# Optimization experiments

Measured on AMD Instinct MI355X. Metric: run time of the kernel, lower is better.

The kernel has to match this reference:

```python
import jax, jax.numpy as jnp
import numpy as np

B, D, N = 2, 256, 8192   # batch, in_channels, sequence length
CI = 128                 # inter_channels
BN_EPS = 1e-5


def conv1x1(w, b, x):
    # w: (Cout, Cin), b: (Cout,), x: (B, Cin, N) -> (B, Cout, N)
    return jnp.einsum('oc,bcn->bon', w, x) + b[None, :, None]


def maxpool2(x):
    # MaxPool1d(kernel_size=2): (B, C, N) -> (B, C, N//2)
    b, c, n = x.shape
    return x.reshape(b, c, n // 2, 2).max(axis=-1)


def setup_inputs() -> dict:
    key = jax.random.key(0)
    ks = jax.random.split(key, 11)
    s_in = 1.0 / np.sqrt(D)
    s_ci = 1.0 / np.sqrt(CI)
    return {
        'f': jax.random.normal(ks[0], (B, D, N), dtype=jnp.float32),
        'g_w': jax.random.uniform(ks[1], (CI, D), jnp.float32, -s_in, s_in),
        'g_b': jax.random.uniform(ks[2], (CI,), jnp.float32, -s_in, s_in),
        'theta_w': jax.random.uniform(ks[3], (CI, D), jnp.float32, -s_in, s_in),
        'theta_b': jax.random.uniform(ks[4], (CI,), jnp.float32, -s_in, s_in),
        'phi_w': jax.random.uniform(ks[5], (CI, D), jnp.float32, -s_in, s_in),
        'phi_b': jax.random.uniform(ks[6], (CI,), jnp.float32, -s_in, s_in),
        'W_w': jax.random.uniform(ks[7], (D, CI), jnp.float32, -s_ci, s_ci),
        'W_b': jax.random.uniform(ks[8], (D,), jnp.float32, -s_ci, s_ci),
        'bn_gamma': jax.random.normal(ks[9], (D,), dtype=jnp.float32) * 0.1,
        'bn_beta': jax.random.normal(ks[10], (D,), dtype=jnp.float32) * 0.1,
    }


def reference(f, g_w, g_b, theta_w, theta_b, phi_w, phi_b, W_w, W_b, bn_gamma, bn_beta):
    # projections (1x1 convs); g and phi are sub-sampled by maxpool(2)
    g_f = maxpool2(conv1x1(g_w, g_b, f))          # (B, CI, N/2)
    theta_f = conv1x1(theta_w, theta_b, f)        # (B, CI, N)
    phi_f = maxpool2(conv1x1(phi_w, phi_b, f))    # (B, CI, N/2)

    # affinity: theta^T @ phi, softmax over keys (no scale, as in source)
    A = jnp.einsum('bcn,bcm->bnm', theta_f, phi_f)     # (B, N, N/2)
    A = jax.nn.softmax(A, axis=-1)
    y = jnp.einsum('bnm,bcm->bcn', A, g_f)             # (B, CI, N)

    # W: 1x1 conv + BatchNorm1d (training-mode batch stats), residual
    Wy = conv1x1(W_w, W_b, y)                          # (B, D, N)
    mean = Wy.mean(axis=(0, 2), keepdims=True)
    var = Wy.var(axis=(0, 2), keepdims=True)           # biased, like torch BN
    Wy = (Wy - mean) * jax.lax.rsqrt(var + BN_EPS)
    Wy = Wy * bn_gamma[None, :, None] + bn_beta[None, :, None]
    return Wy + f
```

## Files before the change

### kernel.cpp

```cpp
#include <hip/hip_runtime.h>
#include <hip/hip_bf16.h>
#include <math.h>

#define B_ 2
#define D_ 256
#define N_ 8192
#define CI_ 128
#define M_ 4096
#define BN_EPS_ 1e-5f
#define LOG2E_ 1.4426950408889634f

#define GLOBAL_AS __attribute__((address_space(1)))
#define LDS_AS __attribute__((address_space(3)))

#define OFF_WALL 0
#define OFF_THT  65536
#define OFF_PHT  (OFF_THT + 1048576)
#define OFF_GT   (OFF_PHT + 524288)
#define OFF_YP   (OFF_GT  + 524288)
#define OFF_ML   (OFF_YP  + 4194304)
#define OFF_MEAN (OFF_ML + 131072)
#define OFF_RSTD (OFF_MEAN + 256)

typedef __attribute__((ext_vector_type(8))) short bfrag;
typedef __attribute__((ext_vector_type(4))) float f4v;
typedef __attribute__((ext_vector_type(16))) float f16v;
typedef __attribute__((ext_vector_type(4))) short s4v;
typedef __attribute__((ext_vector_type(4))) unsigned u4v;

__device__ inline unsigned short bf16rne(float x) {
    unsigned u = __float_as_uint(x);
    u += 0x7fff + ((u >> 16) & 1);
    return (unsigned short)(u >> 16);
}

__device__ inline float exp2fast(float x) {
    float r;
    asm("v_exp_f32 %0, %1" : "=v"(r) : "v"(x));
    return r;
}

__global__ __launch_bounds__(256) void wconv_kernel(
    const float* __restrict__ gw, const float* __restrict__ tw, const float* __restrict__ pw,
    const float* __restrict__ Ww, short* __restrict__ wall)
{
    int idx = blockIdx.x * 256 + threadIdx.x;
    int which = idx >> 15;
    int rem = idx & 32767;
    const float* src = (which == 0) ? gw : (which == 1) ? tw : (which == 2) ? pw : Ww;
    float v = src[rem];
    if (which == 1) v *= LOG2E_;
    wall[idx] = (short)bf16rne(v);
}

__global__ __launch_bounds__(256, 2) void proj_kernel(
    const float* __restrict__ f, const short* __restrict__ wall,
    const float* __restrict__ tb, const float* __restrict__ gb, const float* __restrict__ pb,
    short* __restrict__ th_t, short* __restrict__ g_t, short* __restrict__ ph_t)
{
    __shared__ short sF[32 * 72];

    const int tid = threadIdx.x;
    const int wave = tid >> 6, lane = tid & 63;
    const int lq = lane & 15, quad = lane >> 4;
    const int b = blockIdx.y;
    const int n0 = blockIdx.x * 32;

    const float* fb = f + (size_t)b * D_ * N_;

    f4v acc[6][2];
#pragma unroll
    for (int ct = 0; ct < 6; ct++)
#pragma unroll
        for (int nf = 0; nf < 2; nf++) acc[ct][nf] = (f4v){0.f, 0.f, 0.f, 0.f};

    const int sn = tid & 31;
    const int sgrp = tid >> 5;

    for (int kc = 0; kc < D_; kc += 64) {
        __syncthreads();
#pragma unroll
        for (int jj = 0; jj < 4; jj++) {
            int dd = kc + sgrp * 8 + 2 * jj;
            float v0 = fb[(size_t)dd * N_ + n0 + sn];
            float v1 = fb[(size_t)(dd + 1) * N_ + n0 + sn];
            unsigned pk = (unsigned)bf16rne(v0) | ((unsigned)bf16rne(v1) << 16);
            *(unsigned*)&sF[sn * 72 + sgrp * 8 + 2 * jj] = pk;
        }
        __syncthreads();

        bfrag afr[6][2], bfr[2][2];
#pragma unroll
        for (int ks = 0; ks < 2; ks++) {
#pragma unroll
            for (int nf = 0; nf < 2; nf++)
                bfr[nf][ks] = *(const bfrag*)&sF[(nf * 16 + lq) * 72 + ks * 32 + quad * 8];
#pragma unroll
            for (int ct = 0; ct < 6; ct++)
                afr[ct][ks] = *(const bfrag*)&wall[(wave * 96 + ct * 16 + lq) * 256 + kc + ks * 32 + quad * 8];
        }
#pragma unroll
        for (int ks = 0; ks < 2; ks++)
#pragma unroll
            for (int ct = 0; ct < 6; ct++) {
                acc[ct][0] = __builtin_amdgcn_mfma_f32_16x16x32_bf16(afr[ct][ks], bfr[0][ks], acc[ct][0], 0, 0, 0);
                acc[ct][1] = __builtin_amdgcn_mfma_f32_16x16x32_bf16(afr[ct][ks], bfr[1][ks], acc[ct][1], 0, 0, 0);
            }
    }

#pragma unroll
    for (int ct = 0; ct < 6; ct++) {
        const int cf = wave * 6 + ct;
#pragma unroll
        for (int nf = 0; nf < 2; nf++) {
            f4v v = acc[ct][nf];
            const int n = n0 + nf * 16 + lq;
            if (cf < 8) {
                const int cb = cf * 16 + quad * 4;
                float pl[4];
#pragma unroll
                for (int r = 0; r < 4; r++) {
                    float o = __shfl_xor(v[r], 1);
                    pl[r] = fmaxf(v[r], o) + gb[cb + r];
                }
                if (!(lq & 1)) {
                    const int m = n >> 1;
#pragma unroll
                    for (int r = 0; r < 4; r++)
                        g_t[((size_t)b * CI_ + cb + r) * M_ + m] = (short)bf16rne(pl[r]);
                }
            } else if (cf < 16) {
                const int cb = (cf - 8) * 16 + quad * 4;
                s4v o;
#pragma unroll
                for (int r = 0; r < 4; r++) o[r] = (short)bf16rne(v[r] + tb[cb + r] * LOG2E_);
                *(s4v*)&th_t[((size_t)b * N_ + n) * CI_ + cb] = o;
            } else {
                const int cb = (cf - 16) * 16 + quad * 4;
                float pl[4];
#pragma unroll
                for (int r = 0; r < 4; r++) {
                    float o = __shfl_xor(v[r], 1);
                    pl[r] = fmaxf(v[r], o) + pb[cb + r];
                }
                if (!(lq & 1)) {
                    const int m = n >> 1;
                    s4v o;
#pragma unroll
                    for (int r = 0; r < 4; r++) o[r] = (short)bf16rne(pl[r]);
                    *(s4v*)&ph_t[((size_t)b * M_ + m) * CI_ + cb] = o;
                }
            }
        }
    }
}

__global__ __launch_bounds__(256, 2) void attn_kernel(
    const short* __restrict__ th_p, const short* __restrict__ ph_p,
    const short* __restrict__ g_p, short* __restrict__ yp, float* __restrict__ ml)
{
    __shared__ short sPh[2][64 * 128];

    const int tid = threadIdx.x;
    const int wave = tid >> 6, lane = tid & 63;
    const int l = lane & 31, h = lane >> 5;

    const int bid = blockIdx.x;
    const int b = bid & 1;
    const int split = (bid >> 1) & 3;
    const int q0 = (bid >> 3) * 128;
    const int qg = q0 + wave * 32 + l;

    const short* thr = th_p + ((size_t)b * N_ + qg) * CI_;
    bfrag tf[8];
#pragma unroll
    for (int s = 0; s < 8; s++)
        tf[s] = *(const bfrag*)&thr[s * 16 + h * 8];

    f16v yacc[4];
#pragma unroll
    for (int ct = 0; ct < 4; ct++)
#pragma unroll
        for (int r = 0; r < 16; r++) yacc[ct][r] = 0.f;
    float mI = -INFINITY, lI = 0.f;

    const short* phg = ph_p + (size_t)b * M_ * CI_;
    const short* gg  = g_p + (size_t)b * CI_ * M_;

    const int k0 = split * 1024;
    const int xm = l & 15;

    const int prow = (lane >> 4);
    const int pslot = lane & 15;

#define STAGE_DMA(BUF, KC)                                                                  \
    do {                                                                                    \
        _Pragma("unroll")                                                                   \
        for (int p = 0; p < 4; p++) {                                                       \
            const int rp = wave * 16 + p * 4 + prow;                     \
            const int cg = pslot ^ (p * 4 + prow);                   \
            __builtin_amdgcn_global_load_lds(                                               \
                (const GLOBAL_AS void*)(phg + (size_t)((KC) + rp) * 128 + cg * 8),          \
                (LDS_AS void*)(&sPh[BUF][(wave * 16 + p * 4) * 128]), 16, 0, 0);            \
        }                                                                                   \
    } while (0)

    STAGE_DMA(0, k0);

    int cur = 0;
    for (int kc = k0; kc < k0 + 1024; kc += 64) {
        __syncthreads();
        const bool nxt = (kc + 64 < k0 + 1024);

        bfrag ga[4][4];
#pragma unroll
        for (int ct = 0; ct < 4; ct++)
#pragma unroll
            for (int s = 0; s < 4; s++)
                ga[ct][s] = *(const bfrag*)&gg[(size_t)(ct * 32 + l) * M_ + kc + s * 16 + h * 8];

        if (nxt) STAGE_DMA(cur ^ 1, kc + 64);
        __builtin_amdgcn_sched_barrier(0);

        f16v sv[2];
        __builtin_amdgcn_s_setprio(1);
#pragma unroll
        for (int kt = 0; kt < 2; kt++) {
            f16v a;
#pragma unroll
            for (int r = 0; r < 16; r++) a[r] = 0.f;
#pragma unroll
            for (int s = 0; s < 8; s++) {
                bfrag pa = *(const bfrag*)&sPh[cur][(kt * 32 + l) * 128 + (((s << 1) | h) ^ xm) * 8];
                a = __builtin_amdgcn_mfma_f32_32x32x16_bf16(pa, tf[s], a, 0, 0, 0);
            }
            sv[kt] = a;
        }
        __builtin_amdgcn_s_setprio(0);

        float mx = fmaxf(sv[0][0], sv[1][0]);
#pragma unroll
        for (int r = 1; r < 16; r++) mx = fmaxf(mx, fmaxf(sv[0][r], sv[1][r]));
        mx = fmaxf(mx, __shfl_xor(mx, 32));

        if (__any(mx > mI + 8.f)) {
            float mnew = fmaxf(mI, mx);
            float al = exp2fast(mI - mnew);
            lI *= al;
#pragma unroll
            for (int ct = 0; ct < 4; ct++)
#pragma unroll
                for (int r = 0; r < 16; r++) yacc[ct][r] *= al;
            mI = mnew;
        }

        float ps = 0.f;
        unsigned pw[16];
#pragma unroll
        for (int kt = 0; kt < 2; kt++)
#pragma unroll
            for (int i = 0; i < 8; i++) {
                const int r = 2 * i;
                float p0 = exp2fast(sv[kt][r] - mI);
                float p1 = exp2fast(sv[kt][r + 1] - mI);
                ps += p0 + p1;
                unsigned pk;
                asm("v_cvt_pk_bf16_f32 %0, %1, %2" : "=v"(pk) : "v"(p0), "v"(p1));
                pw[kt * 8 + (i >> 1) * 2 + (i & 1)] = pk;
            }
        ps += __shfl_xor(ps, 32);
        lI += ps;

        bfrag pf[4];
#pragma unroll
        for (int s = 0; s < 4; s++) {
            const int kt = s >> 1;
            const int iA = kt * 8 + ((2 * s) & 3) * 2;
            const int iB = kt * 8 + ((2 * s + 1) & 3) * 2;
            unsigned A0 = pw[iA], A1 = pw[iA + 1];
            unsigned B0 = pw[iB], B1 = pw[iB + 1];
            unsigned O0 = h ? B0 : A0;
            unsigned O1 = h ? B1 : A1;
            unsigned Xs0 = h ? A0 : B0;
            unsigned Xs1 = h ? A1 : B1;
            unsigned X0 = (unsigned)__shfl_xor((int)Xs0, 32);
            unsigned X1 = (unsigned)__shfl_xor((int)Xs1, 32);
            u4v t;
            t.x = h ? X0 : O0;
            t.y = h ? X1 : O1;
            t.z = h ? O0 : X0;
            t.w = h ? O1 : X1;
            pf[s] = __builtin_bit_cast(bfrag, t);
        }

        __builtin_amdgcn_s_setprio(1);
#pragma unroll
        for (int ct = 0; ct < 4; ct++)
#pragma unroll
            for (int s = 0; s < 4; s++)
                yacc[ct] = __builtin_amdgcn_mfma_f32_32x32x16_bf16(ga[ct][s], pf[s], yacc[ct], 0, 0, 0);
        __builtin_amdgcn_s_setprio(0);

        cur ^= 1;
    }
#undef STAGE_DMA

    short* yb = yp + (((size_t)split * B_ + b) * N_) * CI_;
#pragma unroll
    for (int ct = 0; ct < 4; ct++)
#pragma unroll
        for (int rq = 0; rq < 4; rq++) {
            const int c0 = ct * 32 + 8 * rq + 4 * h;
            s4v o;
#pragma unroll
            for (int j = 0; j < 4; j++) o[j] = (short)bf16rne(yacc[ct][rq * 4 + j]);
            *(s4v*)&yb[(size_t)qg * CI_ + c0] = o;
        }
    if (h == 0) {
        float* mlb = ml + ((split * B_ + b) * 2) * N_;
        mlb[qg] = mI;
        mlb[N_ + qg] = lI;
    }
}

__global__ __launch_bounds__(256) void wy_merge_kernel(
    const short* __restrict__ yp, const float* __restrict__ ml,
    const short* __restrict__ wall2, const float* __restrict__ Wb,
    float* __restrict__ out)
{
    const int tid = threadIdx.x;
    const int wave = tid >> 6, lane = tid & 63;
    const int l = lane & 31, h = lane >> 5;
    const int b = blockIdx.y;
    const int n = blockIdx.x * 32 + l;

    float m[4], lv[4];
#pragma unroll
    for (int sp = 0; sp < 4; sp++) {
        const float* mlb = ml + ((sp * B_ + b) * 2) * N_;
        m[sp] = mlb[n];
        lv[sp] = mlb[N_ + n];
    }
    float mmax = fmaxf(fmaxf(m[0], m[1]), fmaxf(m[2], m[3]));
    float e[4], den = 0.f;
#pragma unroll
    for (int sp = 0; sp < 4; sp++) { e[sp] = exp2fast(m[sp] - mmax); den += lv[sp] * e[sp]; }
    float inv = 1.0f / den;
#pragma unroll
    for (int sp = 0; sp < 4; sp++) e[sp] *= inv;

    bfrag by[8];
#pragma unroll
    for (int s = 0; s < 8; s++) {
        float a[8];
#pragma unroll
        for (int j = 0; j < 8; j++) a[j] = 0.f;
#pragma unroll
        for (int sp = 0; sp < 4; sp++) {
            bfrag yv = *(const bfrag*)&yp[(((size_t)sp * B_ + b) * N_ + n) * CI_ + s * 16 + h * 8];
            u4v u = __builtin_bit_cast(u4v, yv);
#pragma unroll
            for (int p = 0; p < 4; p++) {
                a[2 * p]     = fmaf(e[sp], __uint_as_float(u[p] << 16), a[2 * p]);
                a[2 * p + 1] = fmaf(e[sp], __uint_as_float(u[p] & 0xffff0000u), a[2 * p + 1]);
            }
        }
        u4v pk;
#pragma unroll
        for (int p = 0; p < 4; p++) {
            unsigned r;
            asm("v_cvt_pk_bf16_f32 %0, %1, %2" : "=v"(r) : "v"(a[2 * p]), "v"(a[2 * p + 1]));
            pk[p] = r;
        }
        by[s] = __builtin_bit_cast(bfrag, pk);
    }

    f16v acc[2];
#pragma unroll
    for (int rt = 0; rt < 2; rt++)
#pragma unroll
        for (int r = 0; r < 16; r++) acc[rt][r] = 0.f;

#pragma unroll
    for (int s = 0; s < 8; s++)
#pragma unroll
        for (int rt = 0; rt < 2; rt++) {
            bfrag aw = *(const bfrag*)&wall2[((wave * 2 + rt) * 32 + l) * 128 + s * 16 + h * 8];
            acc[rt] = __builtin_amdgcn_mfma_f32_32x32x16_bf16(aw, by[s], acc[rt], 0, 0, 0);
        }

#pragma unroll
    for (int rt = 0; rt < 2; rt++)
#pragma unroll
        for (int r = 0; r < 16; r++) {
            const int d = (wave * 2 + rt) * 32 + (r & 3) + 8 * (r >> 2) + 4 * h;
            out[((size_t)b * D_ + d) * N_ + n] = acc[rt][r] + Wb[d];
        }
}

__global__ __launch_bounds__(256) void stats_kernel(
    const float* __restrict__ wy, float* __restrict__ mean, float* __restrict__ rstd)
{
    __shared__ float ssum[256], ssq[256];
    int d = blockIdx.x;
    int tid = threadIdx.x;
    float s = 0.f, sq = 0.f;
    for (int b = 0; b < B_; b++) {
        const float4* p = (const float4*)(wy + (size_t)b * D_ * N_ + (size_t)d * N_);
        for (int i = tid; i < N_ / 4; i += 256) {
            float4 v = p[i];
            s += v.x + v.y + v.z + v.w;
            sq = fmaf(v.x, v.x, sq);
            sq = fmaf(v.y, v.y, sq);
            sq = fmaf(v.z, v.z, sq);
            sq = fmaf(v.w, v.w, sq);
        }
    }
    ssum[tid] = s; ssq[tid] = sq;
    __syncthreads();
    for (int st = 128; st > 0; st >>= 1) {
        if (tid < st) { ssum[tid] += ssum[tid + st]; ssq[tid] += ssq[tid + st]; }
        __syncthreads();
    }
    if (tid == 0) {
        float inv = 1.0f / (float)(B_ * N_);
        float mn = ssum[0] * inv;
        float var = ssq[0] * inv - mn * mn;
        mean[d] = mn;
        rstd[d] = rsqrtf(var + BN_EPS_);
    }
}

__global__ __launch_bounds__(256) void bn_res_kernel(
    float* __restrict__ out, const float* __restrict__ f,
    const float* __restrict__ mean, const float* __restrict__ rstd,
    const float* __restrict__ gamma, const float* __restrict__ beta)
{
    int i = blockIdx.x * 256 + threadIdx.x;
    size_t e = (size_t)i * 4;
    int d = (int)((e >> 13) & 255);
    float4 wy = ((const float4*)out)[i];
    float4 ff = ((const float4*)f)[i];
    float sc = rstd[d] * gamma[d];
    float mn = mean[d];
    float bt = beta[d];
    float4 r;
    r.x = (wy.x - mn) * sc + bt + ff.x;
    r.y = (wy.y - mn) * sc + bt + ff.y;
    r.z = (wy.z - mn) * sc + bt + ff.z;
    r.w = (wy.w - mn) * sc + bt + ff.w;
    ((float4*)out)[i] = r;
}

extern "C" void kernel_launch(void* const* d_in, const int* in_sizes, int n_in,
                              void* d_out, int out_size, void* d_ws, size_t ws_size,
                              hipStream_t stream)
{
    const float* f   = (const float*)d_in[0];
    const float* g_w = (const float*)d_in[1];
    const float* g_b = (const float*)d_in[2];
    const float* t_w = (const float*)d_in[3];
    const float* t_b = (const float*)d_in[4];
    const float* p_w = (const float*)d_in[5];
    const float* p_b = (const float*)d_in[6];
    const float* W_w = (const float*)d_in[7];
    const float* W_b = (const float*)d_in[8];
    const float* gam = (const float*)d_in[9];
    const float* bet = (const float*)d_in[10];
    float* out = (float*)d_out;
    float* ws = (float*)d_ws;

    short* wall  = (short*)(ws + OFF_WALL);
    short* wall2 = wall + 3 * 32768;
    short* th_t = (short*)(ws + OFF_THT);
    short* ph_t = (short*)(ws + OFF_PHT);
    short* g_t  = (short*)(ws + OFF_GT);
    short* ypart = (short*)(ws + OFF_YP);
    float* mlp = ws + OFF_ML;
    float* mnp = ws + OFF_MEAN;
    float* rsp = ws + OFF_RSTD;

    wconv_kernel<<<512, 256, 0, stream>>>(g_w, t_w, p_w, W_w, wall);
    proj_kernel<<<dim3(N_ / 32, B_), 256, 0, stream>>>(f, wall, t_b, g_b, p_b,
                                                       th_t, g_t, ph_t);
    attn_kernel<<<512, 256, 0, stream>>>(th_t, ph_t, g_t, ypart, mlp);
    wy_merge_kernel<<<dim3(N_ / 32, B_), 256, 0, stream>>>(ypart, mlp, wall2, W_b, out);
    stats_kernel<<<D_, 256, 0, stream>>>(out, mnp, rsp);
    bn_res_kernel<<<(B_ * D_ * N_ / 4) / 256, 256, 0, stream>>>(out, f, mnp, rsp, gam, bet);
}
```

Before: 209.3 us.

## Stage g tiles into LDS via async DMA instead of per-wave global loads

The g operand for the PV matmul was loaded straight from global memory into registers by every wave, so the four waves fetched the same tile four times. It is now staged through a double-buffered LDS tile with padded rows (72 shorts) using global_load_lds, issued alongside the phi prefetch. The goal is to cut redundant global traffic and register pressure and to overlap the g fetch with compute. In exchange LDS use grows, which may lower occupancy, and extra LDS reads are added in the MFMA loop.

```diff
diff --git a/kernel.cpp b/kernel.cpp
--- a/kernel.cpp
+++ b/kernel.cpp
@@ -160,6 +160,7 @@
     const short* __restrict__ g_p, short* __restrict__ yp, float* __restrict__ ml)
 {
     __shared__ short sPh[2][64 * 128];
+    __shared__ short sG [2][128 * 72];
 
     const int tid = threadIdx.x;
     const int wave = tid >> 6, lane = tid & 63;
@@ -192,6 +193,15 @@
 
     const int prow = (lane >> 4);
     const int pslot = lane & 15;
+
+    const int i0 = (wave < 2) ? wave * 5 : 10 + (wave - 2) * 4;
+    const int nIss = (wave < 2) ? 5 : 4;
+    int gsrc[5];
+#pragma unroll
+    for (int p = 0; p < 5; p++) {
+        const int t = (i0 + p) * 64 + lane;
+        gsrc[p] = (t / 9) * M_ + (t % 9) * 8;
+    }
 
 #define STAGE_DMA(BUF, KC)                                                                  \
     do {                                                                                    \
@@ -203,6 +213,13 @@
                 (const GLOBAL_AS void*)(phg + (size_t)((KC) + rp) * 128 + cg * 8),          \
                 (LDS_AS void*)(&sPh[BUF][(wave * 16 + p * 4) * 128]), 16, 0, 0);            \
         }                                                                                   \
+        _Pragma("unroll")                                                                   \
+        for (int p = 0; p < 5; p++) {                                                       \
+            if (p < nIss)                                                                   \
+                __builtin_amdgcn_global_load_lds(                                           \
+                    (const GLOBAL_AS void*)(gg + gsrc[p] + (KC)),                           \
+                    (LDS_AS void*)(&sG[BUF][(i0 + p) * 512]), 16, 0, 0);                    \
+        }                                                                                   \
     } while (0)
 
     STAGE_DMA(0, k0);
@@ -211,16 +228,10 @@
     for (int kc = k0; kc < k0 + 1024; kc += 64) {
         __syncthreads();
         const bool nxt = (kc + 64 < k0 + 1024);
-
-        bfrag ga[4][4];
-#pragma unroll
-        for (int ct = 0; ct < 4; ct++)
-#pragma unroll
-            for (int s = 0; s < 4; s++)
-                ga[ct][s] = *(const bfrag*)&gg[(size_t)(ct * 32 + l) * M_ + kc + s * 16 + h * 8];
-
-        if (nxt) STAGE_DMA(cur ^ 1, kc + 64);
-        __builtin_amdgcn_sched_barrier(0);
+        if (nxt) {
+            STAGE_DMA(cur ^ 1, kc + 64);
+            __builtin_amdgcn_sched_barrier(0);
+        }
 
         f16v sv[2];
         __builtin_amdgcn_s_setprio(1);
@@ -297,8 +308,10 @@
 #pragma unroll
         for (int ct = 0; ct < 4; ct++)
 #pragma unroll
-            for (int s = 0; s < 4; s++)
-                yacc[ct] = __builtin_amdgcn_mfma_f32_32x32x16_bf16(ga[ct][s], pf[s], yacc[ct], 0, 0, 0);
+            for (int s = 0; s < 4; s++) {
+                bfrag ga = *(const bfrag*)&sG[cur][(ct * 32 + l) * 72 + s * 16 + h * 8];
+                yacc[ct] = __builtin_amdgcn_mfma_f32_32x32x16_bf16(ga, pf[s], yacc[ct], 0, 0, 0);
+            }
         __builtin_amdgcn_s_setprio(0);
 
         cur ^= 1;
```

Measured after the change: 180.0 us. 14.0% less time.
